# Kernel optimization log

Measured on AMD Instinct MI355X. Metric: run time of the kernel, lower is better.

The kernel has to match this reference:

```python
import jax, jax.numpy as jnp
import numpy as np

D_MODEL = 1024
D_STATE = 16
D_CONV = 4
EXPAND = 2
D_INNER = EXPAND * D_MODEL  # 2048
DT_RANK = (D_MODEL + 15) // 16  # 64
BATCH = 2
SEQ = 1024


def setup_inputs() -> dict:
    key = jax.random.key(0)
    ks = jax.random.split(key, 9)
    s = 0.02
    x = jax.random.normal(ks[0], (BATCH, SEQ, D_MODEL), jnp.float32)
    W_in = jax.random.normal(ks[1], (D_MODEL, 2 * D_INNER), jnp.float32) * s
    conv_w = jax.random.normal(ks[2], (D_INNER, D_CONV), jnp.float32) * s
    conv_b = jnp.zeros((D_INNER,), jnp.float32)
    W_x = jax.random.normal(ks[3], (D_INNER, DT_RANK + 2 * D_STATE), jnp.float32) * s
    W_dt = jax.random.normal(ks[4], (DT_RANK, D_INNER), jnp.float32) * (DT_RANK ** -0.5)
    # dt bias init: inverse softplus of dt ~ U(1e-3, 0.1)
    dt0 = jax.random.uniform(ks[5], (D_INNER,), jnp.float32, 1e-3, 0.1)
    b_dt = dt0 + jnp.log(-jnp.expm1(-dt0))
    # S4D-real A init: A[d, n] = -(n+1)
    A_log = jnp.log(jnp.tile(jnp.arange(1, D_STATE + 1, dtype=jnp.float32), (D_INNER, 1)))
    D_skip = jnp.ones((D_INNER,), jnp.float32)
    W_out = jax.random.normal(ks[6], (D_INNER, D_MODEL), jnp.float32) * s
    return {"x": x, "W_in": W_in, "conv_w": conv_w, "conv_b": conv_b,
            "W_x": W_x, "W_dt": W_dt, "b_dt": b_dt, "A_log": A_log,
            "D_skip": D_skip, "W_out": W_out}


def _mamba_forward(x, W_in, conv_w, conv_b, W_x, W_dt, b_dt, A_log, D_skip, W_out):
    Bsz, L, _ = x.shape
    # input projection -> [B, L, 2*d_inner], split into stream and gate
    xz = x @ W_in
    xr, z = jnp.split(xz, 2, axis=-1)
    # depthwise causal conv1d over time
    xt = xr.transpose(0, 2, 1)                       # [B, d_inner, L]
    kern = conv_w[:, None, :]                        # [d_inner, 1, d_conv]
    xc = jax.lax.conv_general_dilated(
        xt, kern, window_strides=(1,), padding=[(D_CONV - 1, 0)],
        feature_group_count=D_INNER, dimension_numbers=("NCH", "OIH", "NCH"))
    xc = jax.nn.silu(xc + conv_b[None, :, None]).transpose(0, 2, 1)  # [B, L, d_inner]
    # data-dependent dt, B, C
    dbl = xc @ W_x                                   # [B, L, dt_rank + 2*d_state]
    dt, Bm, Cm = jnp.split(dbl, [DT_RANK, DT_RANK + D_STATE], axis=-1)
    dt = jax.nn.softplus(dt @ W_dt + b_dt)           # [B, L, d_inner]
    A = -jnp.exp(A_log)                              # [d_inner, d_state]

    def step(h, inp):
        dt_t, B_t, C_t, x_t = inp                    # [B,d_inner],[B,d_state],[B,d_state],[B,d_inner]
        dA = jnp.exp(dt_t[..., None] * A)            # [B, d_inner, d_state]
        h = dA * h + (dt_t * x_t)[..., None] * B_t[:, None, :]
        y = jnp.einsum("bds,bs->bd", h, C_t)
        return h, y

    h0 = jnp.zeros((Bsz, D_INNER, D_STATE), x.dtype)
    xs = (dt.transpose(1, 0, 2), Bm.transpose(1, 0, 2),
          Cm.transpose(1, 0, 2), xc.transpose(1, 0, 2))
    _, ys = jax.lax.scan(step, h0, xs)               # ys: [L, B, d_inner]
    y = ys.transpose(1, 0, 2) + xc * D_skip
    y = y * jax.nn.silu(z)
    return y @ W_out                                 # [B, L, d_model]


def reference(x, W_in, conv_w, conv_b, W_x, W_dt, b_dt, A_log, D_skip, W_out):
    return _mamba_forward(x, W_in, conv_w, conv_b, W_x, W_dt, b_dt, A_log, D_skip, W_out)
```

## Files before the change

kernel.cpp:

```cpp
#include <hip/hip_runtime.h>

#define BATCH 2
#define SEQL 1024
#define DMODEL 1024
#define DINNER 2048
#define DSTATE 16
#define DTRANK 64
#define NCH 64
#define LC 16

typedef short bf16x8 __attribute__((ext_vector_type(8)));
typedef float f32x4 __attribute__((ext_vector_type(4)));
typedef int i32x4 __attribute__((ext_vector_type(4)));

__device__ __forceinline__ unsigned short f2bf(float f) {
  unsigned u = __float_as_uint(f);
  return (unsigned short)((u + 0x7fffu + ((u >> 16) & 1u)) >> 16);
}
__device__ __forceinline__ float bf2f(unsigned short u) {
  return __uint_as_float((unsigned)u << 16);
}
__device__ __forceinline__ float sigmoidf_(float x) { return 1.f / (1.f + __expf(-x)); }

__device__ __forceinline__ void gl_lds16(const unsigned short* g, unsigned short* l) {
  __builtin_amdgcn_global_load_lds(
      (const __attribute__((address_space(1))) unsigned int*)g,
      (__attribute__((address_space(3))) unsigned int*)l, 16, 0, 0);
}

__global__ __launch_bounds__(256) void k_gemm_n64(
    const unsigned short* __restrict__ A,
    const unsigned short* __restrict__ Bt,
    float* __restrict__ C, unsigned short* __restrict__ C2,
    int M, int N, int K, const float* __restrict__ bias, int mode)
{
  __shared__ __attribute__((aligned(16))) unsigned short As[128 * 64];
  __shared__ __attribute__((aligned(16))) unsigned short Bs[64 * 64];
  const int tid = threadIdx.x;
  const int wave = tid >> 6, lane = tid & 63;
  const int gx = gridDim.x;
  const int nwg = gx * gridDim.y;
  const int flat = blockIdx.x + gx * blockIdx.y;
  const int sw = (flat & 7) * (nwg >> 3) + (flat >> 3);
  const int m0 = (sw % gx) * 128, n0 = (sw / gx) * 64;
  const int Kc = K / gridDim.z;
  const int k0beg = blockIdx.z * Kc;
  float* Cz = C + (size_t)blockIdx.z * M * N;
  unsigned short* C2z = C2 + (size_t)blockIdx.z * M * N;
  const int wr = (wave & 1) * 64, wc = (wave >> 1) * 32;
  const int fr = lane & 15;
  const int qw = lane >> 4;

  int srowA[4], scolA[4];
  #pragma unroll
  for (int i = 0; i < 4; ++i) {
    int off = wave * 4096 + i * 1024 + lane * 16;
    int row = off >> 7;
    int c16 = ((off >> 4) & 7) ^ (row & 7);
    srowA[i] = row;
    scolA[i] = c16 * 8;
  }
  int srowB[2], scolB[2];
  #pragma unroll
  for (int i = 0; i < 2; ++i) {
    int off = wave * 2048 + i * 1024 + lane * 16;
    int row = off >> 7;
    int c16 = ((off >> 4) & 7) ^ (row & 7);
    srowB[i] = row;
    scolB[i] = c16 * 8;
  }

  f32x4 acc[4][2] = {};
  for (int k0 = k0beg; k0 < k0beg + Kc; k0 += 64) {
    #pragma unroll
    for (int i = 0; i < 4; ++i)
      gl_lds16(A + (size_t)(m0 + srowA[i]) * K + k0 + scolA[i],
               &As[(wave * 4096 + i * 1024) >> 1]);
    #pragma unroll
    for (int i = 0; i < 2; ++i)
      gl_lds16(Bt + (size_t)(n0 + srowB[i]) * K + k0 + scolB[i],
               &Bs[(wave * 2048 + i * 1024) >> 1]);
    __syncthreads();
    #pragma unroll
    for (int t = 0; t < 2; ++t) {
      bf16x8 af[4], bfv[2];
      #pragma unroll
      for (int i = 0; i < 4; ++i) {
        int row = wr + i * 16 + fr;
        int c16 = (t * 4 + qw) ^ (row & 7);
        af[i] = *(const bf16x8*)&As[row * 64 + c16 * 8];
      }
      #pragma unroll
      for (int j = 0; j < 2; ++j) {
        int row = wc + j * 16 + fr;
        int c16 = (t * 4 + qw) ^ (row & 7);
        bfv[j] = *(const bf16x8*)&Bs[row * 64 + c16 * 8];
      }
      #pragma unroll
      for (int i = 0; i < 4; ++i)
        #pragma unroll
        for (int j = 0; j < 2; ++j)
          acc[i][j] = __builtin_amdgcn_mfma_f32_16x16x32_bf16(af[i], bfv[j], acc[i][j], 0, 0, 0);
    }
    __syncthreads();
  }
  const int rr = qw * 4;
  if (mode == 0) {
    #pragma unroll
    for (int i = 0; i < 4; ++i)
      #pragma unroll
      for (int j = 0; j < 2; ++j)
        #pragma unroll
        for (int r = 0; r < 4; ++r)
          Cz[(size_t)(m0 + wr + i * 16 + rr + r) * N + (n0 + wc + j * 16 + fr)] =
              acc[i][j][r];
  } else if (mode == 1) {
    #pragma unroll
    for (int j = 0; j < 2; ++j) {
      float bj = bias[n0 + wc + j * 16 + fr];
      #pragma unroll
      for (int i = 0; i < 4; ++i)
        #pragma unroll
        for (int r = 0; r < 4; ++r) {
          float v = acc[i][j][r] + bj;
          C2[(size_t)(m0 + wr + i * 16 + rr + r) * N + (n0 + wc + j * 16 + fr)] =
              f2bf(__logf(1.f + __expf(v)));
        }
    }
  } else if (mode == 2) {
    #pragma unroll
    for (int i = 0; i < 4; ++i)
      #pragma unroll
      for (int j = 0; j < 2; ++j)
        #pragma unroll
        for (int r = 0; r < 4; ++r)
          C2[(size_t)(m0 + wr + i * 16 + rr + r) * N + (n0 + wc + j * 16 + fr)] =
              f2bf(acc[i][j][r]);
  } else {
    #pragma unroll
    for (int i = 0; i < 4; ++i)
      #pragma unroll
      for (int j = 0; j < 2; ++j)
        #pragma unroll
        for (int r = 0; r < 4; ++r)
          C2z[(size_t)(m0 + wr + i * 16 + rr + r) * N + (n0 + wc + j * 16 + fr)] =
              f2bf(acc[i][j][r]);
  }
}

__device__ __forceinline__ void transpose_tile(
    const float* __restrict__ src, unsigned short* __restrict__ dst,
    int R, int C, int bx, int by, float* t )
{
  int bc = bx * 64, br = by * 64;
  int tr = threadIdx.x >> 2;
  int tc = (threadIdx.x & 3) * 16;
  #pragma unroll
  for (int i = 0; i < 4; ++i) {
    float4 v = *(const float4*)(src + (size_t)(br + tr) * C + bc + tc + i * 4);
    t[tr * 65 + tc + i * 4 + 0] = v.x; t[tr * 65 + tc + i * 4 + 1] = v.y;
    t[tr * 65 + tc + i * 4 + 2] = v.z; t[tr * 65 + tc + i * 4 + 3] = v.w;
  }
  __syncthreads();
  unsigned short tmp[16];
  #pragma unroll
  for (int i = 0; i < 16; ++i) tmp[i] = f2bf(t[(tc + i) * 65 + tr]);
  unsigned short* dp = dst + (size_t)(bc + tr) * R + br + tc;
  *(i32x4*)dp = *(i32x4*)&tmp[0];
  *(i32x4*)(dp + 8) = *(i32x4*)&tmp[8];
}

__global__ __launch_bounds__(256) void k_prep1(
    const float* __restrict__ x,   unsigned short* __restrict__ xbf,
    const float* __restrict__ Win, unsigned short* __restrict__ wint)
{
  __shared__ float t[64 * 65];
  int bid = blockIdx.x;
  if (bid < 1024) {
    int i = (bid * 256 + threadIdx.x) * 8;
    float4 a = *(const float4*)(x + i);
    float4 b = *(const float4*)(x + i + 4);
    unsigned short tmp[8] = {f2bf(a.x), f2bf(a.y), f2bf(a.z), f2bf(a.w),
                             f2bf(b.x), f2bf(b.y), f2bf(b.z), f2bf(b.w)};
    *(i32x4*)(xbf + i) = *(i32x4*)tmp;
  } else {
    int tt = bid - 1024;
    transpose_tile(Win, wint, 1024, 4096, tt & 63, tt >> 6, t);
  }
}

__global__ __launch_bounds__(256) void k_conv_prep(
    const unsigned short* __restrict__ xzb, const float* __restrict__ cw,
    const float* __restrict__ cb, unsigned short* __restrict__ xcb,
    const float* __restrict__ Wout, unsigned short* __restrict__ woutt,
    const float* __restrict__ Wdt,  unsigned short* __restrict__ wdtt,
    const float* __restrict__ Wx,   unsigned short* __restrict__ wxt)
{
  __shared__ float t[64 * 65];
  int bid = blockIdx.x;
  if (bid < 2048) {
    int idx = (bid * 256 + threadIdx.x) * 8;
    int d0 = idx & (DINNER - 1);
    int bl = idx >> 11;
    int l = bl & (SEQL - 1);
    float s[8];
    {
      float4 c0 = *(const float4*)(cb + d0);
      float4 c1 = *(const float4*)(cb + d0 + 4);
      s[0] = c0.x; s[1] = c0.y; s[2] = c0.z; s[3] = c0.w;
      s[4] = c1.x; s[5] = c1.y; s[6] = c1.z; s[7] = c1.w;
    }
    float4 w[8];
    #pragma unroll
    for (int i = 0; i < 8; ++i) w[i] = *(const float4*)(cw + (d0 + i) * 4);
    #pragma unroll
    for (int k = 0; k < 4; ++k) {
      int ll = l - 3 + k;
      if (ll >= 0) {
        bf16x8 v = *(const bf16x8*)&xzb[(size_t)(bl - 3 + k) * 4096 + d0];
        #pragma unroll
        for (int i = 0; i < 8; ++i)
          s[i] += bf2f((unsigned short)v[i]) * ((const float*)&w[i])[k];
      }
    }
    unsigned short o[8];
    #pragma unroll
    for (int i = 0; i < 8; ++i) {
      float r = s[i] * sigmoidf_(s[i]);
      o[i] = f2bf(r);
    }
    *(i32x4*)&xcb[idx] = *(i32x4*)o;
  } else if (bid < 2560) {
    int tt = bid - 2048;
    transpose_tile(Wout, woutt, 2048, 1024, tt & 15, tt >> 4, t);
  } else if (bid < 2592) {
    int tt = bid - 2560;
    transpose_tile(Wdt, wdtt, 64, 2048, tt, 0, t);
  } else {
    int idx = (bid - 2592) * 256 + threadIdx.x;
    int k = idx & (DINNER - 1);
    int n = idx >> 11;
    float v = (n < 96) ? Wx[(size_t)k * 96 + n] : 0.f;
    wxt[idx] = f2bf(v);
  }
}

__global__ void k_reduce2(const float* __restrict__ part, float* __restrict__ dbl,
                          unsigned short* __restrict__ dtraw)
{
  int idx = (blockIdx.x * 256 + threadIdx.x) * 4;
  f32x4 s = *(const f32x4*)(part + idx);
  #pragma unroll
  for (int z = 1; z < 8; ++z) s += *(const f32x4*)(part + (size_t)z * 2048 * 128 + idx);
  *(f32x4*)(dbl + idx) = s;
  int col = idx & 127, rw = idx >> 7;
  if (col < 64) {
    unsigned short tmp[4] = {f2bf(s[0]), f2bf(s[1]), f2bf(s[2]), f2bf(s[3])};
    *(unsigned long long*)(dtraw + rw * 64 + col) = *(unsigned long long*)tmp;
  }
}

__global__ void k_reduce5(const unsigned short* __restrict__ part, float* __restrict__ out)
{
  int idx = (blockIdx.x * 256 + threadIdx.x) * 8;
  float s[8] = {};
  #pragma unroll
  for (int z = 0; z < 2; ++z) {
    bf16x8 v = *(const bf16x8*)(part + (size_t)z * 2048 * 1024 + idx);
    #pragma unroll
    for (int i = 0; i < 8; ++i) s[i] += bf2f((unsigned short)v[i]);
  }
  *(f32x4*)(out + idx) = *(f32x4*)&s[0];
  *(f32x4*)(out + idx + 4) = *(f32x4*)&s[4];
}

__global__ __launch_bounds__(256) void k_scan_A(
    const unsigned short* __restrict__ dtb, const unsigned short* __restrict__ xcb,
    const float* __restrict__ dbl, const float* __restrict__ Alog,
    unsigned short* __restrict__ hendb, float* __restrict__ sumdtb)
{
  __shared__ __attribute__((aligned(16))) float bcB[LC][DSTATE];
  int gid = blockIdx.x * 256 + threadIdx.x;
  int d = gid & (DINNER - 1);
  int t = gid >> 11;
  int c = t & (NCH - 1);
  int b = t >> 6;
  const int r0 = b * SEQL + c * LC;
  bcB[threadIdx.x >> 4][threadIdx.x & 15] =
      dbl[(size_t)(r0 + (threadIdx.x >> 4)) * 128 + 64 + (threadIdx.x & 15)];
  float As[DSTATE];
  #pragma unroll
  for (int i = 0; i < 4; ++i) {
    f32x4 a = *(const f32x4*)&Alog[d * DSTATE + i * 4];
    #pragma unroll
    for (int j = 0; j < 4; ++j) As[i * 4 + j] = -__expf(a[j]);
  }
  __syncthreads();
  float h[DSTATE];
  #pragma unroll
  for (int s = 0; s < DSTATE; ++s) h[s] = 0.f;
  float sumdt = 0.f;
  #pragma unroll
  for (int li = 0; li < LC; li += 2) {
    float dt0 = bf2f(dtb[(size_t)(r0 + li) * DINNER + d]);
    float xv0 = bf2f(xcb[(size_t)(r0 + li) * DINNER + d]);
    float dt1 = bf2f(dtb[(size_t)(r0 + li + 1) * DINNER + d]);
    float xv1 = bf2f(xcb[(size_t)(r0 + li + 1) * DINNER + d]);
    f32x4 B0[4], B1[4];
    #pragma unroll
    for (int i = 0; i < 4; ++i) B0[i] = *(const f32x4*)&bcB[li][i * 4];
    #pragma unroll
    for (int i = 0; i < 4; ++i) B1[i] = *(const f32x4*)&bcB[li + 1][i * 4];
    float dtx0 = dt0 * xv0, dtx1 = dt1 * xv1;
    sumdt += dt0 + dt1;
    const float* Bv0 = (const float*)B0;
    const float* Bv1 = (const float*)B1;
    #pragma unroll
    for (int s = 0; s < DSTATE; ++s) {
      float dA0 = __expf(dt0 * As[s]);
      h[s] = dA0 * h[s] + dtx0 * Bv0[s];
      float dA1 = __expf(dt1 * As[s]);
      h[s] = dA1 * h[s] + dtx1 * Bv1[s];
    }
  }
  size_t base = ((size_t)(b * NCH + c) * DSTATE) * DINNER + d;
  #pragma unroll
  for (int s = 0; s < DSTATE; ++s) hendb[base + (size_t)s * DINNER] = f2bf(h[s]);
  sumdtb[(size_t)(b * NCH + c) * DINNER + d] = sumdt;
}

__global__ void k_scan_B(const unsigned short* __restrict__ hendb,
                         const float* __restrict__ sumdtb,
                         const float* __restrict__ Alog,
                         unsigned short* __restrict__ hinb)
{
  int gid = blockIdx.x * 256 + threadIdx.x;
  int d = gid & (DINNER - 1);
  int s = (gid >> 11) & (DSTATE - 1);
  int b = gid >> 15;
  const float As = -__expf(Alog[d * DSTATE + s]);
  float h = 0.f;
  for (int c0 = 0; c0 < NCH; c0 += 16) {
    float he[16], sd[16];
    #pragma unroll
    for (int i = 0; i < 16; ++i) {
      he[i] = bf2f(hendb[((size_t)(b * NCH + c0 + i) * DSTATE + s) * DINNER + d]);
      sd[i] = sumdtb[(size_t)(b * NCH + c0 + i) * DINNER + d];
    }
    #pragma unroll
    for (int i = 0; i < 16; ++i) {
      hinb[((size_t)(b * NCH + c0 + i) * DSTATE + s) * DINNER + d] = f2bf(h);
      h = __expf(sd[i] * As) * h + he[i];
    }
  }
}

__global__ __launch_bounds__(256) void k_scan_C(
    const unsigned short* __restrict__ dtb, const unsigned short* __restrict__ xcb,
    const float* __restrict__ dbl, const float* __restrict__ Alog,
    const unsigned short* __restrict__ hinb, const float* __restrict__ Dskip,
    const unsigned short* __restrict__ xzb, unsigned short* __restrict__ yact)
{
  __shared__ __attribute__((aligned(16))) float bc[LC][32];
  int gid = blockIdx.x * 256 + threadIdx.x;
  int d = gid & (DINNER - 1);
  int t = gid >> 11;
  int c = t & (NCH - 1);
  int b = t >> 6;
  const int r0 = b * SEQL + c * LC;
  {
    int step = threadIdx.x >> 4, j = (threadIdx.x & 15) * 2;
    float2 v = *(const float2*)&dbl[(size_t)(r0 + step) * 128 + 64 + j];
    bc[step][j] = v.x; bc[step][j + 1] = v.y;
  }
  float As[DSTATE];
  #pragma unroll
  for (int i = 0; i < 4; ++i) {
    f32x4 a = *(const f32x4*)&Alog[d * DSTATE + i * 4];
    #pragma unroll
    for (int j = 0; j < 4; ++j) As[i * 4 + j] = -__expf(a[j]);
  }
  float h[DSTATE];
  size_t base = ((size_t)(b * NCH + c) * DSTATE) * DINNER + d;
  #pragma unroll
  for (int s = 0; s < DSTATE; ++s) h[s] = bf2f(hinb[base + (size_t)s * DINNER]);
  const float dsk = Dskip[d];
  __syncthreads();
  #pragma unroll
  for (int li = 0; li < LC; li += 2) {
    const int r = r0 + li;
    float dt0 = bf2f(dtb[(size_t)r * DINNER + d]);
    float xv0 = bf2f(xcb[(size_t)r * DINNER + d]);
    float zv0 = bf2f(xzb[(size_t)r * 4096 + 2048 + d]);
    float dt1 = bf2f(dtb[(size_t)(r + 1) * DINNER + d]);
    float xv1 = bf2f(xcb[(size_t)(r + 1) * DINNER + d]);
    float zv1 = bf2f(xzb[(size_t)(r + 1) * 4096 + 2048 + d]);
    f32x4 B0[4], C0[4], B1[4], C1[4];
    #pragma unroll
    for (int i = 0; i < 4; ++i) B0[i] = *(const f32x4*)&bc[li][i * 4];
    #pragma unroll
    for (int i = 0; i < 4; ++i) C0[i] = *(const f32x4*)&bc[li][16 + i * 4];
    #pragma unroll
    for (int i = 0; i < 4; ++i) B1[i] = *(const f32x4*)&bc[li + 1][i * 4];
    #pragma unroll
    for (int i = 0; i < 4; ++i) C1[i] = *(const f32x4*)&bc[li + 1][16 + i * 4];
    const float* Bv0 = (const float*)B0; const float* Cv0 = (const float*)C0;
    const float* Bv1 = (const float*)B1; const float* Cv1 = (const float*)C1;
    float dtx0 = dt0 * xv0, dtx1 = dt1 * xv1;
    float y0 = 0.f, y1 = 0.f;
    #pragma unroll
    for (int s = 0; s < DSTATE; ++s) {
      float dA0 = __expf(dt0 * As[s]);
      h[s] = dA0 * h[s] + dtx0 * Bv0[s];
      y0 += h[s] * Cv0[s];
      float dA1 = __expf(dt1 * As[s]);
      h[s] = dA1 * h[s] + dtx1 * Bv1[s];
      y1 += h[s] * Cv1[s];
    }
    y0 += xv0 * dsk;
    y1 += xv1 * dsk;
    float ya0 = y0 * (zv0 * sigmoidf_(zv0));
    float ya1 = y1 * (zv1 * sigmoidf_(zv1));
    yact[(size_t)r * DINNER + d] = f2bf(ya0);
    yact[(size_t)(r + 1) * DINNER + d] = f2bf(ya1);
  }
}

extern "C" void kernel_launch(void* const* d_in, const int* in_sizes, int n_in,
                              void* d_out, int out_size, void* d_ws, size_t ws_size,
                              hipStream_t stream) {
  const float* x     = (const float*)d_in[0];
  const float* Win   = (const float*)d_in[1];
  const float* cw    = (const float*)d_in[2];
  const float* cbias = (const float*)d_in[3];
  const float* Wx    = (const float*)d_in[4];
  const float* Wdt   = (const float*)d_in[5];
  const float* bdt   = (const float*)d_in[6];
  const float* Alog  = (const float*)d_in[7];
  const float* Dsk   = (const float*)d_in[8];
  const float* Wout  = (const float*)d_in[9];
  float* out = (float*)d_out;

  char* ws = (char*)d_ws;
  const size_t MB = 1 << 20;
  unsigned short* xzb   = (unsigned short*)(ws);
  unsigned short* xbf   = (unsigned short*)(ws + 16 * MB);
  unsigned short* wint  = (unsigned short*)(ws + 20 * MB);
  unsigned short* xcb   = (unsigned short*)(ws + 28 * MB);
  unsigned short* wxt   = (unsigned short*)(ws + 36 * MB);
  float*          dbl   = (float*)         (ws + 37 * MB);
  unsigned short* dtraw = (unsigned short*)(ws + 38 * MB);
  unsigned short* wdtt  = (unsigned short*)(ws + 39 * MB);
  unsigned short* dtb16 = (unsigned short*)(ws + 40 * MB);
  unsigned short* hendb = (unsigned short*)(ws + 48 * MB);
  float*          sumdt = (float*)         (ws + 56 * MB);
  unsigned short* hinb  = (unsigned short*)(ws + 57 * MB);
  unsigned short* yact  = (unsigned short*)(ws + 65 * MB);
  unsigned short* woutt = (unsigned short*)(ws + 73 * MB);
  float*          part2 = (float*)         (ws + 77 * MB);
  unsigned short* part5 = (unsigned short*)(ws + 85 * MB);
  (void)ws_size; (void)in_sizes; (void)n_in; (void)out_size;

  k_prep1<<<2048, 256, 0, stream>>>(x, xbf, Win, wint);
  k_gemm_n64<<<dim3(16, 64, 1), 256, 0, stream>>>(xbf, wint, nullptr, xzb, 2048, 4096, 1024, nullptr, 2);
  k_conv_prep<<<3616, 256, 0, stream>>>(xzb, cw, cbias, xcb, Wout, woutt, Wdt, wdtt, Wx, wxt);
  k_gemm_n64<<<dim3(16, 2, 8), 256, 0, stream>>>(xcb, wxt, part2, nullptr, 2048, 128, 2048, nullptr, 0);
  k_reduce2<<<256, 256, 0, stream>>>(part2, dbl, dtraw);
  k_gemm_n64<<<dim3(16, 32, 1), 256, 0, stream>>>(dtraw, wdtt, nullptr, dtb16, 2048, 2048, 64, bdt, 1);
  k_scan_A<<<1024, 256, 0, stream>>>(dtb16, xcb, dbl, Alog, hendb, sumdt);
  k_scan_B<<<256, 256, 0, stream>>>(hendb, sumdt, Alog, hinb);
  k_scan_C<<<1024, 256, 0, stream>>>(dtb16, xcb, dbl, Alog, hinb, Dsk, xzb, yact);
  k_gemm_n64<<<dim3(16, 16, 2), 256, 0, stream>>>(yact, woutt, nullptr, part5, 2048, 1024, 2048, nullptr, 3);
  k_reduce5<<<1024, 256, 0, stream>>>(part5, out);
}
```

Measured before the change: 135.5 us.

## Replace split-K partial buffers and reduce kernels with fp32 atomic accumulation

The split-K GEMMs for the x-projection and the output projection now atomically add fp32 partials straight into zero-initialised output buffers. The zeroing is folded into the first prep kernel, which removes two reduction kernels and their partial-buffer traffic. A new dt GEMM kernel reads the fp32 dbl buffer directly and converts it to bf16 while staging into LDS, which drops the dtraw intermediate. The cost is atomic contention on the global stores and non-deterministic summation order.

```diff
diff --git a/kernel.cpp b/kernel.cpp
--- a/kernel.cpp
+++ b/kernel.cpp
@@ -45,8 +45,6 @@
   const int m0 = (sw % gx) * 128, n0 = (sw / gx) * 64;
   const int Kc = K / gridDim.z;
   const int k0beg = blockIdx.z * Kc;
-  float* Cz = C + (size_t)blockIdx.z * M * N;
-  unsigned short* C2z = C2 + (size_t)blockIdx.z * M * N;
   const int wr = (wave & 1) * 64, wc = (wave >> 1) * 32;
   const int fr = lane & 15;
   const int qw = lane >> 4;
@@ -105,16 +103,7 @@
     __syncthreads();
   }
   const int rr = qw * 4;
-  if (mode == 0) {
-    #pragma unroll
-    for (int i = 0; i < 4; ++i)
-      #pragma unroll
-      for (int j = 0; j < 2; ++j)
-        #pragma unroll
-        for (int r = 0; r < 4; ++r)
-          Cz[(size_t)(m0 + wr + i * 16 + rr + r) * N + (n0 + wc + j * 16 + fr)] =
-              acc[i][j][r];
-  } else if (mode == 1) {
+  if (mode == 1) {
     #pragma unroll
     for (int j = 0; j < 2; ++j) {
       float bj = bias[n0 + wc + j * 16 + fr];
@@ -143,8 +132,85 @@
       for (int j = 0; j < 2; ++j)
         #pragma unroll
         for (int r = 0; r < 4; ++r)
-          C2z[(size_t)(m0 + wr + i * 16 + rr + r) * N + (n0 + wc + j * 16 + fr)] =
-              f2bf(acc[i][j][r]);
+          atomicAdd(&C[(size_t)(m0 + wr + i * 16 + rr + r) * N + (n0 + wc + j * 16 + fr)],
+                    acc[i][j][r]);
+  }
+}
+
+__global__ __launch_bounds__(256) void k_gemm_dt(
+    const float* __restrict__ dblsrc,
+    const unsigned short* __restrict__ Bt,
+    unsigned short* __restrict__ C2,
+    const float* __restrict__ bias)
+{
+  __shared__ __attribute__((aligned(16))) unsigned short As[128 * 64];
+  __shared__ __attribute__((aligned(16))) unsigned short Bs[64 * 64];
+  const int tid = threadIdx.x;
+  const int wave = tid >> 6, lane = tid & 63;
+  const int gx = gridDim.x;
+  const int nwg = gx * gridDim.y;
+  const int flat = blockIdx.x + gx * blockIdx.y;
+  const int sw = (flat & 7) * (nwg >> 3) + (flat >> 3);
+  const int m0 = (sw % gx) * 128, n0 = (sw / gx) * 64;
+  const int wr = (wave & 1) * 64, wc = (wave >> 1) * 32;
+  const int fr = lane & 15;
+  const int qw = lane >> 4;
+
+  #pragma unroll
+  for (int i = 0; i < 4; ++i) {
+    int off = wave * 4096 + i * 1024 + lane * 16;
+    int row = off >> 7;
+    int c16 = ((off >> 4) & 7) ^ (row & 7);
+    const float* src = dblsrc + (size_t)(m0 + row) * 128 + c16 * 8;
+    f32x4 u0 = *(const f32x4*)src;
+    f32x4 u1 = *(const f32x4*)(src + 4);
+    unsigned short tmp[8] = {f2bf(u0[0]), f2bf(u0[1]), f2bf(u0[2]), f2bf(u0[3]),
+                             f2bf(u1[0]), f2bf(u1[1]), f2bf(u1[2]), f2bf(u1[3])};
+    *(i32x4*)&As[off >> 1] = *(i32x4*)tmp;
+  }
+  #pragma unroll
+  for (int i = 0; i < 2; ++i) {
+    int off = wave * 2048 + i * 1024 + lane * 16;
+    int row = off >> 7;
+    int c16 = ((off >> 4) & 7) ^ (row & 7);
+    gl_lds16(Bt + (size_t)(n0 + row) * 64 + c16 * 8,
+             &Bs[(wave * 2048 + i * 1024) >> 1]);
+  }
+  __syncthreads();
+  f32x4 acc[4][2] = {};
+  #pragma unroll
+  for (int t = 0; t < 2; ++t) {
+    bf16x8 af[4], bfv[2];
+    #pragma unroll
+    for (int i = 0; i < 4; ++i) {
+      int row = wr + i * 16 + fr;
+      int c16 = (t * 4 + qw) ^ (row & 7);
+      af[i] = *(const bf16x8*)&As[row * 64 + c16 * 8];
+    }
+    #pragma unroll
+    for (int j = 0; j < 2; ++j) {
+      int row = wc + j * 16 + fr;
+      int c16 = (t * 4 + qw) ^ (row & 7);
+      bfv[j] = *(const bf16x8*)&Bs[row * 64 + c16 * 8];
+    }
+    #pragma unroll
+    for (int i = 0; i < 4; ++i)
+      #pragma unroll
+      for (int j = 0; j < 2; ++j)
+        acc[i][j] = __builtin_amdgcn_mfma_f32_16x16x32_bf16(af[i], bfv[j], acc[i][j], 0, 0, 0);
+  }
+  const int rr = qw * 4;
+  #pragma unroll
+  for (int j = 0; j < 2; ++j) {
+    float bj = bias[n0 + wc + j * 16 + fr];
+    #pragma unroll
+    for (int i = 0; i < 4; ++i)
+      #pragma unroll
+      for (int r = 0; r < 4; ++r) {
+        float v = acc[i][j][r] + bj;
+        C2[(size_t)(m0 + wr + i * 16 + rr + r) * 2048 + (n0 + wc + j * 16 + fr)] =
+            f2bf(__logf(1.f + __expf(v)));
+      }
   }
 }
 
@@ -172,7 +238,8 @@
 
 __global__ __launch_bounds__(256) void k_prep1(
     const float* __restrict__ x,   unsigned short* __restrict__ xbf,
-    const float* __restrict__ Win, unsigned short* __restrict__ wint)
+    const float* __restrict__ Win, unsigned short* __restrict__ wint,
+    float* __restrict__ outz, float* __restrict__ dblz)
 {
   __shared__ float t[64 * 65];
   int bid = blockIdx.x;
@@ -183,9 +250,17 @@
     unsigned short tmp[8] = {f2bf(a.x), f2bf(a.y), f2bf(a.z), f2bf(a.w),
                              f2bf(b.x), f2bf(b.y), f2bf(b.z), f2bf(b.w)};
     *(i32x4*)(xbf + i) = *(i32x4*)tmp;
-  } else {
+  } else if (bid < 2048) {
     int tt = bid - 1024;
     transpose_tile(Win, wint, 1024, 4096, tt & 63, tt >> 6, t);
+  } else if (bid < 4096) {
+    int i = ((bid - 2048) * 256 + threadIdx.x) * 4;
+    f32x4 z = {};
+    *(f32x4*)(outz + i) = z;
+  } else {
+    int i = ((bid - 4096) * 256 + threadIdx.x) * 4;
+    f32x4 z = {};
+    *(f32x4*)(dblz + i) = z;
   }
 }
 
@@ -243,35 +318,6 @@
     float v = (n < 96) ? Wx[(size_t)k * 96 + n] : 0.f;
     wxt[idx] = f2bf(v);
   }
-}
-
-__global__ void k_reduce2(const float* __restrict__ part, float* __restrict__ dbl,
-                          unsigned short* __restrict__ dtraw)
-{
-  int idx = (blockIdx.x * 256 + threadIdx.x) * 4;
-  f32x4 s = *(const f32x4*)(part + idx);
-  #pragma unroll
-  for (int z = 1; z < 8; ++z) s += *(const f32x4*)(part + (size_t)z * 2048 * 128 + idx);
-  *(f32x4*)(dbl + idx) = s;
-  int col = idx & 127, rw = idx >> 7;
-  if (col < 64) {
-    unsigned short tmp[4] = {f2bf(s[0]), f2bf(s[1]), f2bf(s[2]), f2bf(s[3])};
-    *(unsigned long long*)(dtraw + rw * 64 + col) = *(unsigned long long*)tmp;
-  }
-}
-
-__global__ void k_reduce5(const unsigned short* __restrict__ part, float* __restrict__ out)
-{
-  int idx = (blockIdx.x * 256 + threadIdx.x) * 8;
-  float s[8] = {};
-  #pragma unroll
-  for (int z = 0; z < 2; ++z) {
-    bf16x8 v = *(const bf16x8*)(part + (size_t)z * 2048 * 1024 + idx);
-    #pragma unroll
-    for (int i = 0; i < 8; ++i) s[i] += bf2f((unsigned short)v[i]);
-  }
-  *(f32x4*)(out + idx) = *(f32x4*)&s[0];
-  *(f32x4*)(out + idx + 4) = *(f32x4*)&s[4];
 }
 
 __global__ __launch_bounds__(256) void k_scan_A(
@@ -449,7 +495,6 @@
   unsigned short* xcb   = (unsigned short*)(ws + 28 * MB);
   unsigned short* wxt   = (unsigned short*)(ws + 36 * MB);
   float*          dbl   = (float*)         (ws + 37 * MB);
-  unsigned short* dtraw = (unsigned short*)(ws + 38 * MB);
   unsigned short* wdtt  = (unsigned short*)(ws + 39 * MB);
   unsigned short* dtb16 = (unsigned short*)(ws + 40 * MB);
   unsigned short* hendb = (unsigned short*)(ws + 48 * MB);
@@ -457,19 +502,15 @@
   unsigned short* hinb  = (unsigned short*)(ws + 57 * MB);
   unsigned short* yact  = (unsigned short*)(ws + 65 * MB);
   unsigned short* woutt = (unsigned short*)(ws + 73 * MB);
-  float*          part2 = (float*)         (ws + 77 * MB);
-  unsigned short* part5 = (unsigned short*)(ws + 85 * MB);
   (void)ws_size; (void)in_sizes; (void)n_in; (void)out_size;
 
-  k_prep1<<<2048, 256, 0, stream>>>(x, xbf, Win, wint);
+  k_prep1<<<4352, 256, 0, stream>>>(x, xbf, Win, wint, out, dbl);
   k_gemm_n64<<<dim3(16, 64, 1), 256, 0, stream>>>(xbf, wint, nullptr, xzb, 2048, 4096, 1024, nullptr, 2);
   k_conv_prep<<<3616, 256, 0, stream>>>(xzb, cw, cbias, xcb, Wout, woutt, Wdt, wdtt, Wx, wxt);
-  k_gemm_n64<<<dim3(16, 2, 8), 256, 0, stream>>>(xcb, wxt, part2, nullptr, 2048, 128, 2048, nullptr, 0);
-  k_reduce2<<<256, 256, 0, stream>>>(part2, dbl, dtraw);
-  k_gemm_n64<<<dim3(16, 32, 1), 256, 0, stream>>>(dtraw, wdtt, nullptr, dtb16, 2048, 2048, 64, bdt, 1);
+  k_gemm_n64<<<dim3(16, 2, 8), 256, 0, stream>>>(xcb, wxt, dbl, nullptr, 2048, 128, 2048, nullptr, 4);
+  k_gemm_dt<<<dim3(16, 32), 256, 0, stream>>>(dbl, wdtt, dtb16, bdt);
   k_scan_A<<<1024, 256, 0, stream>>>(dtb16, xcb, dbl, Alog, hendb, sumdt);
   k_scan_B<<<256, 256, 0, stream>>>(hendb, sumdt, Alog, hinb);
   k_scan_C<<<1024, 256, 0, stream>>>(dtb16, xcb, dbl, Alog, hinb, Dsk, xzb, yact);
-  k_gemm_n64<<<dim3(16, 16, 2), 256, 0, stream>>>(yact, woutt, nullptr, part5, 2048, 1024, 2048, nullptr, 3);
-  k_reduce5<<<1024, 256, 0, stream>>>(part5, out);
-}
+  k_gemm_n64<<<dim3(16, 16, 2), 256, 0, stream>>>(yact, woutt, out, nullptr, 2048, 1024, 2048, nullptr, 4);
+}
```

New measurement: 142.5 us. 5.2% more time.
